# Optimization experiments

Measured on AMD Instinct MI355X. Metric: run time of the kernel, lower is better.

Reference implementation:

```python
import jax, jax.numpy as jnp
import numpy as np

VOCAB = 10000
N_STATE = 384
N_HEAD = 6
N_CTX = 448
B = 128
T = 448  # seq len, must be <= N_CTX


def setup_inputs() -> dict:
    key = jax.random.key(0)
    ks = jax.random.split(key, 10)
    def w(k, shape, scale=0.02):
        return jax.random.normal(k, shape, dtype=jnp.float32) * scale
    return {
        "x": jax.random.randint(ks[0], (B, T), 0, VOCAB),
        "emb": w(ks[1], (VOCAB, N_STATE)),
        "Wq": w(ks[2], (N_STATE, N_STATE)), "bq": w(ks[3], (N_STATE,)),
        "Wk": w(ks[4], (N_STATE, N_STATE)),  # key layer has no bias
        "Wv": w(ks[5], (N_STATE, N_STATE)), "bv": w(ks[6], (N_STATE,)),
        "Wo": w(ks[7], (N_STATE, N_STATE)), "bo": w(ks[8], (N_STATE,)),
    }


def reference(x, emb, Wq, bq, Wk, Wv, bv, Wo, bo):
    b, t = x.shape
    d = N_STATE // N_HEAD  # 64
    scale = d ** (-0.25)

    h = emb[x]                          # [b, t, n_state] embedding lookup
    q = h @ Wq.T + bq                   # [b, t, n_state]
    k = h @ Wk.T                        # key linear has no bias
    v = h @ Wv.T + bv

    # split heads: [b, t, H, d]
    qh = q.reshape(b, t, N_HEAD, d) * scale
    kh = k.reshape(b, t, N_HEAD, d) * scale
    vh = v.reshape(b, t, N_HEAD, d)

    qk = jnp.einsum('bqhd,bkhd->bhqk', qh, kh)          # [b, H, t, t]
    mask = jnp.triu(jnp.full((t, t), -jnp.inf, dtype=qk.dtype), 1)
    qk = qk + mask                                      # causal mask add
    w = jax.nn.softmax(qk.astype(jnp.float32), axis=-1).astype(q.dtype)

    wv = jnp.einsum('bhqk,bkhd->bqhd', w, vh).reshape(b, t, N_STATE)
    out = wv @ Wo.T + bo
    return (out, k, v)
```

## Files before the change

kernel.cpp:

```cpp
#include <hip/hip_runtime.h>
#include <hip/hip_bf16.h>
#include <stdint.h>

typedef __bf16 bf16x8 __attribute__((ext_vector_type(8)));
typedef short short8v __attribute__((ext_vector_type(8)));
typedef float f32x4 __attribute__((ext_vector_type(4)));

#define B_     128
#define T_     448
#define NS     384
#define NH     6
#define HD     64
#define VOCAB_ 10000
#define NOUT   22020096

#define OFF_WQ   0
#define OFF_WK   147456
#define OFF_WV   294912
#define OFF_WO   442368
#define OFF_QTAB 589824
#define OFF_KTAB 4429824
#define OFF_VTAB 8269824
#define OFF_CTX  12109824

__device__ __forceinline__ unsigned short f2bf(float f) {
    union { float f; uint32_t u; } v; v.f = f;
    return (unsigned short)((v.u + 0x7FFFu + ((v.u >> 16) & 1u)) >> 16);
}
__device__ __forceinline__ float bf2f(unsigned short u) {
    union { uint32_t u; float f; } v; v.u = (uint32_t)u << 16;
    return v.f;
}

__global__ __launch_bounds__(256) void k_prep(
    const float* __restrict__ Wq, const float* __restrict__ Wk,
    const float* __restrict__ Wv, const float* __restrict__ Wo,
    unsigned short* __restrict__ ws)
{
    const float* srcs[4] = {Wq, Wk, Wv, Wo};
    const int seg = blockIdx.y;
    int i = (blockIdx.x * 256 + threadIdx.x) * 4;
    if (i >= 147456) return;
    float4 v = *(const float4*)(srcs[seg] + i);
    ushort4 o;
    o.x = f2bf(v.x); o.y = f2bf(v.y); o.z = f2bf(v.z); o.w = f2bf(v.w);
    *(ushort4*)(ws + seg * 147456 + i) = o;
}

__global__ __launch_bounds__(256) void k_table(
    const float* __restrict__ emb, const unsigned short* __restrict__ ws,
    const float* __restrict__ bq, const float* __restrict__ bv,
    unsigned short* __restrict__ wso)
{
    const int p  = blockIdx.y;
    const int v0 = blockIdx.x * 64;
    const int tid = threadIdx.x;
    const int lane = tid & 63, wv = tid >> 6;

    __shared__ __align__(16) unsigned short sA[64][392];

    {
        int r = tid >> 2;
        int srow = min(v0 + r, VOCAB_ - 1);
        const float* src = emb + (size_t)srow * NS + (tid & 3) * 8;
        unsigned short* dst = &sA[r][(tid & 3) * 8];
        #pragma unroll
        for (int j = 0; j < 12; ++j) {
            float4 a0 = *(const float4*)(src + j * 32);
            float4 a1 = *(const float4*)(src + j * 32 + 4);
            ushort4 o0, o1;
            o0.x = f2bf(a0.x); o0.y = f2bf(a0.y); o0.z = f2bf(a0.z); o0.w = f2bf(a0.w);
            o1.x = f2bf(a1.x); o1.y = f2bf(a1.y); o1.z = f2bf(a1.z); o1.w = f2bf(a1.w);
            *(ushort4*)(dst + j * 32) = o0;
            *(ushort4*)(dst + j * 32 + 4) = o1;
        }
    }
    __syncthreads();

    f32x4 acc[4][6];
    #pragma unroll
    for (int i = 0; i < 4; ++i)
        #pragma unroll
        for (int j = 0; j < 6; ++j) acc[i][j] = (f32x4){0.f, 0.f, 0.f, 0.f};

    const int colA = lane & 15;
    const int kb = (lane >> 4) * 8;
    const unsigned short* wlane =
        ws + (size_t)p * 147456 + (size_t)(wv * 96 + colA) * NS + kb;

    #pragma unroll 2
    for (int kc = 0; kc < 12; ++kc) {
        bf16x8 a[4], b[6];
        #pragma unroll
        for (int mf = 0; mf < 4; ++mf)
            a[mf] = *(const bf16x8*)&sA[mf * 16 + colA][kc * 32 + kb];
        #pragma unroll
        for (int nf = 0; nf < 6; ++nf)
            b[nf] = *(const bf16x8*)(wlane + (size_t)(nf * 16) * NS + kc * 32);
        #pragma unroll
        for (int mf = 0; mf < 4; ++mf)
            #pragma unroll
            for (int nf = 0; nf < 6; ++nf)
                acc[mf][nf] = __builtin_amdgcn_mfma_f32_16x16x32_bf16(
                    a[mf], b[nf], acc[mf][nf], 0, 0, 0);
    }

    const int r0 = (lane >> 4) * 4;
    const float scale = 0.35355339059327373f;

    if (p == 0) {
        unsigned short* qt_ = wso + OFF_QTAB;
        #pragma unroll
        for (int nf = 0; nf < 6; ++nf) {
            int n = wv * 96 + nf * 16 + colA;
            float bias = bq[n];
            #pragma unroll
            for (int mf = 0; mf < 4; ++mf)
                #pragma unroll
                for (int r = 0; r < 4; ++r) {
                    int row = v0 + mf * 16 + r0 + r;
                    if (row < VOCAB_)
                        qt_[(size_t)row * NS + n] = f2bf((acc[mf][nf][r] + bias) * scale);
                }
        }
    } else if (p == 1) {
        unsigned short* kt_ = wso + OFF_KTAB;
        #pragma unroll
        for (int nf = 0; nf < 6; ++nf) {
            int n = wv * 96 + nf * 16 + colA;
            #pragma unroll
            for (int mf = 0; mf < 4; ++mf)
                #pragma unroll
                for (int r = 0; r < 4; ++r) {
                    int row = v0 + mf * 16 + r0 + r;
                    if (row < VOCAB_)
                        kt_[(size_t)row * NS + n] = f2bf(acc[mf][nf][r] * scale);
                }
        }
    } else {
        unsigned short* vt_ = wso + OFF_VTAB;
        #pragma unroll
        for (int nf = 0; nf < 6; ++nf) {
            int n = wv * 96 + nf * 16 + colA;
            float bias = bv[n];
            #pragma unroll
            for (int mf = 0; mf < 4; ++mf)
                #pragma unroll
                for (int r = 0; r < 4; ++r) {
                    int row = v0 + mf * 16 + r0 + r;
                    if (row < VOCAB_)
                        vt_[(size_t)row * NS + n] = f2bf(acc[mf][nf][r] + bias);
                }
        }
    }
}

__global__ __launch_bounds__(256) void k_attn(
    const int* __restrict__ x, const unsigned short* __restrict__ ws,
    unsigned short* __restrict__ ctxb)
{
    const int bid = blockIdx.x;
    const int qt = bid % 7;
    const int h  = (bid / 7) % NH;
    const int b  = bid / (7 * NH);
    const int tid = threadIdx.x;
    const int lane = tid & 63, wv = tid >> 6;

    __shared__ __align__(16) unsigned short sK[64][72];
    __shared__ __align__(16) unsigned short sVT[64][72];
    __shared__ __align__(16) unsigned short sP[4][16][72];

    const int* xb = x + (size_t)b * T_;
    const unsigned short* qtab = ws + OFF_QTAB;
    const unsigned short* ktab = ws + OFF_KTAB;
    const unsigned short* vtab = ws + OFF_VTAB;

    const int qrow = qt * 64 + wv * 16 + (lane & 15);
    const int qtok = xb[qrow];
    const unsigned short* qbase =
        qtab + (size_t)qtok * NS + h * HD + (lane >> 4) * 8;
    bf16x8 qf0 = *(const bf16x8*)qbase;
    bf16x8 qf1 = *(const bf16x8*)(qbase + 32);

    f32x4 o[4];
    #pragma unroll
    for (int nf = 0; nf < 4; ++nf) o[nf] = (f32x4){0.f, 0.f, 0.f, 0.f};
    float lsum[4] = {0.f, 0.f, 0.f, 0.f};

    const int tk = tid >> 2;
    const int cc = (tid & 3) * 16;
    const int vd = tid & 63;
    const int vg = tid >> 6;

    for (int kv = 0; kv <= qt; ++kv) {
        __syncthreads();
        {
            int tkn = xb[kv * 64 + tk];
            const unsigned short* kset = ktab + (size_t)tkn * NS + h * HD + cc;
            *(short8v*)&sK[tk][cc]     = *(const short8v*)kset;
            *(short8v*)&sK[tk][cc + 8] = *(const short8v*)(kset + 8);
        }
        {
            unsigned short tv[16];
            #pragma unroll
            for (int j = 0; j < 16; ++j) {
                int t = xb[kv * 64 + vg * 16 + j];
                tv[j] = vtab[(size_t)t * NS + h * HD + vd];
            }
            *(short8v*)&sVT[vd][vg * 16]     = *(const short8v*)&tv[0];
            *(short8v*)&sVT[vd][vg * 16 + 8] = *(const short8v*)&tv[8];
        }
        __syncthreads();

        f32x4 s[4];
        #pragma unroll
        for (int nf = 0; nf < 4; ++nf) s[nf] = (f32x4){0.f, 0.f, 0.f, 0.f};
        #pragma unroll
        for (int nf = 0; nf < 4; ++nf) {
            bf16x8 kb0 = *(const bf16x8*)&sK[nf * 16 + (lane & 15)][(lane >> 4) * 8];
            s[nf] = __builtin_amdgcn_mfma_f32_16x16x32_bf16(qf0, kb0, s[nf], 0, 0, 0);
            bf16x8 kb1 = *(const bf16x8*)&sK[nf * 16 + (lane & 15)][32 + (lane >> 4) * 8];
            s[nf] = __builtin_amdgcn_mfma_f32_16x16x32_bf16(qf1, kb1, s[nf], 0, 0, 0);
        }

        if (kv == qt) {
            const int rloc = wv * 16 + (lane >> 4) * 4;
            const int cloc = lane & 15;
            #pragma unroll
            for (int nf = 0; nf < 4; ++nf)
                #pragma unroll
                for (int r = 0; r < 4; ++r) {
                    float sv = (cloc + nf * 16 > rloc + r) ? -1e30f : s[nf][r];
                    float p = __expf(sv);
                    s[nf][r] = p;
                    lsum[r] += p;
                }
        } else {
            #pragma unroll
            for (int nf = 0; nf < 4; ++nf)
                #pragma unroll
                for (int r = 0; r < 4; ++r) {
                    float p = __expf(s[nf][r]);
                    s[nf][r] = p;
                    lsum[r] += p;
                }
        }

        #pragma unroll
        for (int nf = 0; nf < 4; ++nf)
            #pragma unroll
            for (int r = 0; r < 4; ++r)
                sP[wv][(lane >> 4) * 4 + r][nf * 16 + (lane & 15)] = f2bf(s[nf][r]);
        asm volatile("s_waitcnt lgkmcnt(0)" ::: "memory");

        bf16x8 pa0 = *(const bf16x8*)&sP[wv][lane & 15][(lane >> 4) * 8];
        bf16x8 pa1 = *(const bf16x8*)&sP[wv][lane & 15][32 + (lane >> 4) * 8];
        #pragma unroll
        for (int nf = 0; nf < 4; ++nf) {
            bf16x8 vb0 = *(const bf16x8*)&sVT[nf * 16 + (lane & 15)][(lane >> 4) * 8];
            o[nf] = __builtin_amdgcn_mfma_f32_16x16x32_bf16(pa0, vb0, o[nf], 0, 0, 0);
            bf16x8 vb1 = *(const bf16x8*)&sVT[nf * 16 + (lane & 15)][32 + (lane >> 4) * 8];
            o[nf] = __builtin_amdgcn_mfma_f32_16x16x32_bf16(pa1, vb1, o[nf], 0, 0, 0);
        }
    }

    float inv[4];
    #pragma unroll
    for (int r = 0; r < 4; ++r) {
        float l = lsum[r];
        #pragma unroll
        for (int off = 1; off < 16; off <<= 1)
            l += __shfl_xor(l, off, 16);
        inv[r] = 1.0f / l;
    }

    #pragma unroll
    for (int nf = 0; nf < 4; ++nf) {
        int col = h * HD + nf * 16 + (lane & 15);
        #pragma unroll
        for (int r = 0; r < 4; ++r) {
            int rowg = qt * 64 + wv * 16 + (lane >> 4) * 4 + r;
            ctxb[((size_t)b * T_ + rowg) * NS + col] = f2bf(o[nf][r] * inv[r]);
        }
    }
}

__global__ __launch_bounds__(256) void k_gather(
    const int* __restrict__ x, const unsigned short* __restrict__ ws,
    float* __restrict__ out_k, float* __restrict__ out_v)
{
    int i = blockIdx.x * 256 + threadIdx.x;
    int row = i / 48;
    int c = (i - row * 48) * 8;
    int tok = x[row];
    const unsigned short* ks = ws + OFF_KTAB + (size_t)tok * NS + c;
    const unsigned short* vs = ws + OFF_VTAB + (size_t)tok * NS + c;
    ushort4 k0 = *(const ushort4*)ks;
    ushort4 k1 = *(const ushort4*)(ks + 4);
    ushort4 v0 = *(const ushort4*)vs;
    ushort4 v1 = *(const ushort4*)(vs + 4);
    const float inv = 2.8284271247461903f;
    float4 fk0 = {bf2f(k0.x) * inv, bf2f(k0.y) * inv, bf2f(k0.z) * inv, bf2f(k0.w) * inv};
    float4 fk1 = {bf2f(k1.x) * inv, bf2f(k1.y) * inv, bf2f(k1.z) * inv, bf2f(k1.w) * inv};
    float4 fv0 = {bf2f(v0.x), bf2f(v0.y), bf2f(v0.z), bf2f(v0.w)};
    float4 fv1 = {bf2f(v1.x), bf2f(v1.y), bf2f(v1.z), bf2f(v1.w)};
    size_t base = (size_t)row * NS + c;
    *(float4*)(out_k + base)     = fk0;
    *(float4*)(out_k + base + 4) = fk1;
    *(float4*)(out_v + base)     = fv0;
    *(float4*)(out_v + base + 4) = fv1;
}

__global__ __launch_bounds__(256) void k_oproj(
    const unsigned short* __restrict__ ws, const float* __restrict__ bo,
    float* __restrict__ out)
{
    const int m0 = blockIdx.x * 64;
    const int tid = threadIdx.x;
    const int lane = tid & 63, wv = tid >> 6;

    __shared__ __align__(16) unsigned short sA[64][392];

    const unsigned short* ctxb = ws + OFF_CTX;

    {
        int r = tid >> 2, seg = tid & 3;
        const unsigned short* src = ctxb + (size_t)(m0 + r) * NS + seg * 96;
        unsigned short* dst = &sA[r][seg * 96];
        #pragma unroll
        for (int j = 0; j < 12; ++j)
            *(short8v*)(dst + j * 8) = *(const short8v*)(src + j * 8);
    }
    __syncthreads();

    f32x4 acc[4][6];
    #pragma unroll
    for (int i = 0; i < 4; ++i)
        #pragma unroll
        for (int j = 0; j < 6; ++j) acc[i][j] = (f32x4){0.f, 0.f, 0.f, 0.f};

    const int colA = lane & 15;
    const int kb = (lane >> 4) * 8;
    const unsigned short* wlane =
        ws + OFF_WO + (size_t)(wv * 96 + colA) * NS + kb;

    #pragma unroll 2
    for (int kc = 0; kc < 12; ++kc) {
        bf16x8 a[4], bfr[6];
        #pragma unroll
        for (int mf = 0; mf < 4; ++mf)
            a[mf] = *(const bf16x8*)&sA[mf * 16 + colA][kc * 32 + kb];
        #pragma unroll
        for (int nf = 0; nf < 6; ++nf)
            bfr[nf] = *(const bf16x8*)(wlane + (size_t)(nf * 16) * NS + kc * 32);
        #pragma unroll
        for (int mf = 0; mf < 4; ++mf)
            #pragma unroll
            for (int nf = 0; nf < 6; ++nf)
                acc[mf][nf] = __builtin_amdgcn_mfma_f32_16x16x32_bf16(
                    a[mf], bfr[nf], acc[mf][nf], 0, 0, 0);
    }

    const int r0 = (lane >> 4) * 4;
    #pragma unroll
    for (int nf = 0; nf < 6; ++nf) {
        int n = wv * 96 + nf * 16 + colA;
        float bias = bo[n];
        #pragma unroll
        for (int mf = 0; mf < 4; ++mf)
            #pragma unroll
            for (int r = 0; r < 4; ++r)
                out[(size_t)(m0 + mf * 16 + r0 + r) * NS + n] = acc[mf][nf][r] + bias;
    }
}

extern "C" void kernel_launch(void* const* d_in, const int* in_sizes, int n_in,
                              void* d_out, int out_size, void* d_ws, size_t ws_size,
                              hipStream_t stream) {
    const int*   x   = (const int*)d_in[0];
    const float* emb = (const float*)d_in[1];
    const float* Wq  = (const float*)d_in[2];
    const float* bq  = (const float*)d_in[3];
    const float* Wk  = (const float*)d_in[4];
    const float* Wv  = (const float*)d_in[5];
    const float* bv  = (const float*)d_in[6];
    const float* Wo  = (const float*)d_in[7];
    const float* bo  = (const float*)d_in[8];

    float* out   = (float*)d_out;
    float* out_k = out + NOUT;
    float* out_v = out + 2 * (size_t)NOUT;
    unsigned short* ws = (unsigned short*)d_ws;

    k_prep<<<dim3(144, 4), 256, 0, stream>>>(Wq, Wk, Wv, Wo, ws);
    k_table<<<dim3(157, 3), 256, 0, stream>>>(emb, ws, bq, bv, ws);
    k_attn<<<dim3(B_ * NH * 7), 256, 0, stream>>>(x, ws, ws + OFF_CTX);
    k_gather<<<dim3(10752), 256, 0, stream>>>(x, ws, out_k, out_v);
    k_oproj<<<dim3(896), 256, 0, stream>>>(ws, bo, out);
}
```

Baseline: 207.8 us.

## Fuse K/V gather into attention kernel and prefetch next KV tile into registers

Merges the separate gather kernel into the attention launch by interleaving gather blocks with attention blocks (two gather blocks per attention block), so the bandwidth-bound output writes run alongside the compute-bound attention instead of after it. It also software-pipelines the attention KV loop: the next tile's K and V rows are loaded into registers while MFMAs run on the current tile in shared memory. This removes one kernel launch and hides global-load latency, at the cost of more live registers and a heterogeneous grid that may change occupancy.

```diff
diff --git a/kernel.cpp b/kernel.cpp
--- a/kernel.cpp
+++ b/kernel.cpp
@@ -22,6 +22,9 @@
 #define OFF_KTAB 4429824
 #define OFF_VTAB 8269824
 #define OFF_CTX  12109824
+
+#define NATT (B_ * NH * 7)
+#define NGAT 10752
 
 __device__ __forceinline__ unsigned short f2bf(float f) {
     union { float f; uint32_t u; } v; v.f = f;
@@ -155,11 +158,40 @@
     }
 }
 
-__global__ __launch_bounds__(256) void k_attn(
+__global__ __launch_bounds__(256) void k_attn_gather(
     const int* __restrict__ x, const unsigned short* __restrict__ ws,
-    unsigned short* __restrict__ ctxb)
+    unsigned short* __restrict__ ctxb,
+    float* __restrict__ out_k, float* __restrict__ out_v)
 {
-    const int bid = blockIdx.x;
+    const int gid = blockIdx.x;
+    const int r3 = gid % 3;
+    const int q3 = gid / 3;
+
+    if (r3 != 0) {
+        int i = (2 * q3 + (r3 - 1)) * 256 + threadIdx.x;
+        int row = i / 48;
+        int c = (i - row * 48) * 8;
+        int tok = x[row];
+        const unsigned short* ks = ws + OFF_KTAB + (size_t)tok * NS + c;
+        const unsigned short* vs = ws + OFF_VTAB + (size_t)tok * NS + c;
+        ushort4 k0 = *(const ushort4*)ks;
+        ushort4 k1 = *(const ushort4*)(ks + 4);
+        ushort4 v0 = *(const ushort4*)vs;
+        ushort4 v1 = *(const ushort4*)(vs + 4);
+        const float inv = 2.8284271247461903f;
+        float4 fk0 = {bf2f(k0.x) * inv, bf2f(k0.y) * inv, bf2f(k0.z) * inv, bf2f(k0.w) * inv};
+        float4 fk1 = {bf2f(k1.x) * inv, bf2f(k1.y) * inv, bf2f(k1.z) * inv, bf2f(k1.w) * inv};
+        float4 fv0 = {bf2f(v0.x), bf2f(v0.y), bf2f(v0.z), bf2f(v0.w)};
+        float4 fv1 = {bf2f(v1.x), bf2f(v1.y), bf2f(v1.z), bf2f(v1.w)};
+        size_t base = (size_t)row * NS + c;
+        *(float4*)(out_k + base)     = fk0;
+        *(float4*)(out_k + base + 4) = fk1;
+        *(float4*)(out_v + base)     = fv0;
+        *(float4*)(out_v + base + 4) = fv1;
+        return;
+    }
+
+    const int bid = q3;
     const int qt = bid % 7;
     const int h  = (bid / 7) % NH;
     const int b  = bid / (7 * NH);
@@ -192,25 +224,40 @@
     const int vd = tid & 63;
     const int vg = tid >> 6;
 
+    short8v kr0, kr1;
+    unsigned short tv[16];
+    {
+        int tkn = xb[tk];
+        const unsigned short* kset = ktab + (size_t)tkn * NS + h * HD + cc;
+        kr0 = *(const short8v*)kset;
+        kr1 = *(const short8v*)(kset + 8);
+        #pragma unroll
+        for (int j = 0; j < 16; ++j) {
+            int t = xb[vg * 16 + j];
+            tv[j] = vtab[(size_t)t * NS + h * HD + vd];
+        }
+    }
+
     for (int kv = 0; kv <= qt; ++kv) {
         __syncthreads();
-        {
-            int tkn = xb[kv * 64 + tk];
+        *(short8v*)&sK[tk][cc]           = kr0;
+        *(short8v*)&sK[tk][cc + 8]       = kr1;
+        *(short8v*)&sVT[vd][vg * 16]     = *(const short8v*)&tv[0];
+        *(short8v*)&sVT[vd][vg * 16 + 8] = *(const short8v*)&tv[8];
+        __syncthreads();
+
+        if (kv < qt) {
+            int base = (kv + 1) * 64;
+            int tkn = xb[base + tk];
             const unsigned short* kset = ktab + (size_t)tkn * NS + h * HD + cc;
-            *(short8v*)&sK[tk][cc]     = *(const short8v*)kset;
-            *(short8v*)&sK[tk][cc + 8] = *(const short8v*)(kset + 8);
-        }
-        {
-            unsigned short tv[16];
+            kr0 = *(const short8v*)kset;
+            kr1 = *(const short8v*)(kset + 8);
             #pragma unroll
             for (int j = 0; j < 16; ++j) {
-                int t = xb[kv * 64 + vg * 16 + j];
+                int t = xb[base + vg * 16 + j];
                 tv[j] = vtab[(size_t)t * NS + h * HD + vd];
             }
-            *(short8v*)&sVT[vd][vg * 16]     = *(const short8v*)&tv[0];
-            *(short8v*)&sVT[vd][vg * 16 + 8] = *(const short8v*)&tv[8];
-        }
-        __syncthreads();
+        }
 
         f32x4 s[4];
         #pragma unroll
@@ -283,32 +330,6 @@
             ctxb[((size_t)b * T_ + rowg) * NS + col] = f2bf(o[nf][r] * inv[r]);
         }
     }
-}
-
-__global__ __launch_bounds__(256) void k_gather(
-    const int* __restrict__ x, const unsigned short* __restrict__ ws,
-    float* __restrict__ out_k, float* __restrict__ out_v)
-{
-    int i = blockIdx.x * 256 + threadIdx.x;
-    int row = i / 48;
-    int c = (i - row * 48) * 8;
-    int tok = x[row];
-    const unsigned short* ks = ws + OFF_KTAB + (size_t)tok * NS + c;
-    const unsigned short* vs = ws + OFF_VTAB + (size_t)tok * NS + c;
-    ushort4 k0 = *(const ushort4*)ks;
-    ushort4 k1 = *(const ushort4*)(ks + 4);
-    ushort4 v0 = *(const ushort4*)vs;
-    ushort4 v1 = *(const ushort4*)(vs + 4);
-    const float inv = 2.8284271247461903f;
-    float4 fk0 = {bf2f(k0.x) * inv, bf2f(k0.y) * inv, bf2f(k0.z) * inv, bf2f(k0.w) * inv};
-    float4 fk1 = {bf2f(k1.x) * inv, bf2f(k1.y) * inv, bf2f(k1.z) * inv, bf2f(k1.w) * inv};
-    float4 fv0 = {bf2f(v0.x), bf2f(v0.y), bf2f(v0.z), bf2f(v0.w)};
-    float4 fv1 = {bf2f(v1.x), bf2f(v1.y), bf2f(v1.z), bf2f(v1.w)};
-    size_t base = (size_t)row * NS + c;
-    *(float4*)(out_k + base)     = fk0;
-    *(float4*)(out_k + base + 4) = fk1;
-    *(float4*)(out_v + base)     = fv0;
-    *(float4*)(out_v + base + 4) = fv1;
 }
 
 __global__ __launch_bounds__(256) void k_oproj(
@@ -394,7 +415,7 @@
 
     k_prep<<<dim3(144, 4), 256, 0, stream>>>(Wq, Wk, Wv, Wo, ws);
     k_table<<<dim3(157, 3), 256, 0, stream>>>(emb, ws, bq, bv, ws);
-    k_attn<<<dim3(B_ * NH * 7), 256, 0, stream>>>(x, ws, ws + OFF_CTX);
-    k_gather<<<dim3(10752), 256, 0, stream>>>(x, ws, out_k, out_v);
+    k_attn_gather<<<dim3(NATT * 3), 256, 0, stream>>>(x, ws, ws + OFF_CTX,
+                                                      out_k, out_v);
     k_oproj<<<dim3(896), 256, 0, stream>>>(ws, bo, out);
 }
```

New measurement: 196.0 us. 1.06x faster.
